# Optimization experiments

Measured on AMD Instinct MI355X. Metric: run time of the kernel, lower is better.

## Reference

```python
import jax, jax.numpy as jnp
import numpy as np

BATCH = 32768
NUM_CLASSES = 1000

def setup_inputs() -> dict:
    key = jax.random.key(0)
    k1, k2 = jax.random.split(key)
    input = jax.random.normal(k1, (BATCH, NUM_CLASSES), dtype=jnp.float32)
    target = jax.random.randint(k2, (BATCH, NUM_CLASSES), 0, 2, dtype=jnp.int32)
    return {"input": input, "target": target}

def reference(input, target):
    # LSEP: loss = log(1 + sum_{i} sum_{p in pos_i} sum_{n in neg_i} exp(x[i,n] - x[i,p]))
    # The pair sum factorizes per sample:
    #   sum_{p,n} exp(x_n - x_p) = (sum_{n in neg} exp(x_n)) * (sum_{p in pos} exp(-x_p))
    pos = target > 0
    neg = target == 0
    s_neg = jnp.sum(jnp.where(neg, jnp.exp(input), 0.0), axis=1)   # [B]
    s_pos = jnp.sum(jnp.where(pos, jnp.exp(-input), 0.0), axis=1)  # [B]
    total = jnp.sum(s_neg * s_pos)
    return jnp.log1p(total).reshape(1).astype(jnp.float32)
```

## Files before the change

### kernel.cpp

```cpp
#include <hip/hip_runtime.h>
#include <math.h>

#define BATCH   32768
#define NCLS    1000
#define NC4     250
#define NBLOCKS 2048
#define NWAVES  (NBLOCKS * 4)
#define RPW     (BATCH / NWAVES)

__device__ __forceinline__ void acc4(float4 xv, int4 tv, float& sn, float& sp) {
    float e0 = __expf(tv.x == 0 ? xv.x : -xv.x);
    float e1 = __expf(tv.y == 0 ? xv.y : -xv.y);
    float e2 = __expf(tv.z == 0 ? xv.z : -xv.z);
    float e3 = __expf(tv.w == 0 ? xv.w : -xv.w);
    sn += (tv.x == 0) ? e0 : 0.0f;  sp += (tv.x == 0) ? 0.0f : e0;
    sn += (tv.y == 0) ? e1 : 0.0f;  sp += (tv.y == 0) ? 0.0f : e1;
    sn += (tv.z == 0) ? e2 : 0.0f;  sp += (tv.z == 0) ? 0.0f : e2;
    sn += (tv.w == 0) ? e3 : 0.0f;  sp += (tv.w == 0) ? 0.0f : e3;
}

__global__ __launch_bounds__(256) void lsep_row_kernel(
    const float* __restrict__ x,
    const int*   __restrict__ t,
    float* __restrict__ wave_out) {

    const int tid   = threadIdx.x;
    const int lane  = tid & 63;
    const int gwave = blockIdx.x * 4 + (tid >> 6);

    const bool tail = (lane + 192 < NC4);

    const float4* xp = (const float4*)x + (size_t)gwave * NC4;
    const int4*   tp = (const int4*)t + (size_t)gwave * NC4;
    const size_t rstep = (size_t)NWAVES * NC4;

    float4 xv0, xv1, xv2, xv3;
    int4   tv0, tv1, tv2, tv3;

    xv0 = xp[lane];       tv0 = tp[lane];
    xv1 = xp[lane + 64];  tv1 = tp[lane + 64];
    xv2 = xp[lane + 128]; tv2 = tp[lane + 128];
    if (tail) { xv3 = xp[lane + 192]; tv3 = tp[lane + 192]; }

    float acc = 0.0f;

    #pragma unroll
    for (int r = 0; r < RPW; ++r) {
        const bool more = (r + 1 < RPW);
        const float4* xn = xp + (size_t)(r + 1) * rstep;
        const int4*   tn = tp + (size_t)(r + 1) * rstep;

        float sn = 0.0f, sp = 0.0f;

        {
            float4 xc = xv0; int4 tc = tv0;
            if (more) { xv0 = xn[lane]; tv0 = tn[lane]; }
            acc4(xc, tc, sn, sp);
        }
        {
            float4 xc = xv1; int4 tc = tv1;
            if (more) { xv1 = xn[lane + 64]; tv1 = tn[lane + 64]; }
            acc4(xc, tc, sn, sp);
        }
        {
            float4 xc = xv2; int4 tc = tv2;
            if (more) { xv2 = xn[lane + 128]; tv2 = tn[lane + 128]; }
            acc4(xc, tc, sn, sp);
        }
        if (tail) {
            float4 xc = xv3; int4 tc = tv3;
            if (more) { xv3 = xn[lane + 192]; tv3 = tn[lane + 192]; }
            acc4(xc, tc, sn, sp);
        }

        #pragma unroll
        for (int off = 32; off > 0; off >>= 1) {
            sn += __shfl_down(sn, off, 64);
            sp += __shfl_down(sp, off, 64);
        }

        if (lane == 0) acc += sn * sp;
    }

    if (lane == 0) wave_out[gwave] = acc;
}

__global__ __launch_bounds__(256) void lsep_reduce_kernel(
    const float* __restrict__ wave_out,
    float* __restrict__ out) {

    const int tid = threadIdx.x;
    const float4* r4 = (const float4*)wave_out;

    float4 a[8];
    #pragma unroll
    for (int j = 0; j < 8; ++j)
        a[j] = r4[tid + 256 * j];

    float v = 0.0f;
    #pragma unroll
    for (int j = 0; j < 8; ++j)
        v += (a[j].x + a[j].y) + (a[j].z + a[j].w);

    #pragma unroll
    for (int off = 32; off > 0; off >>= 1)
        v += __shfl_down(v, off, 64);

    __shared__ float sv[4];
    const int wave = tid >> 6;
    const int lane = tid & 63;
    if (lane == 0) sv[wave] = v;
    __syncthreads();

    if (tid == 0) {
        float total = (sv[0] + sv[1]) + (sv[2] + sv[3]);
        out[0] = log1pf(total);
    }
}

extern "C" void kernel_launch(void* const* d_in, const int* in_sizes, int n_in,
                              void* d_out, int out_size, void* d_ws, size_t ws_size,
                              hipStream_t stream) {
    const float* x = (const float*)d_in[0];
    const int*   t = (const int*)d_in[1];
    float* out     = (float*)d_out;
    float* wave_ws = (float*)d_ws;

    lsep_row_kernel<<<NBLOCKS, 256, 0, stream>>>(x, t, wave_ws);
    lsep_reduce_kernel<<<1, 256, 0, stream>>>(wave_ws, out);
}
```

Baseline: 271.2 us.

## Stream row chunks through LDS with global_load_lds and a 4-deep pipeline

Loads of input and target chunks now go directly from global memory into per-wave LDS buffers via global_load_lds. A software pipeline keeps three chunks in flight, gated by explicit s_waitcnt vmcnt counts. The aim is to raise memory-level parallelism and cut the VGPRs spent holding prefetched registers, and launch bounds now request 5 blocks per CU. In exchange it uses 32 KB of LDS per block and relies on hand-counted vmcnt waits. The code also reads LDS written by the load-to-LDS path without an explicit lgkm wait or barrier.

```diff
diff --git a/kernel.cpp b/kernel.cpp
--- a/kernel.cpp
+++ b/kernel.cpp
@@ -7,6 +7,11 @@
 #define NBLOCKS 2048
 #define NWAVES  (NBLOCKS * 4)
 #define RPW     (BATCH / NWAVES)
+
+typedef const __attribute__((address_space(1))) unsigned int gu32;
+typedef __attribute__((address_space(3)))       unsigned int lu32;
+
+#define WAITVM(N) asm volatile("s_waitcnt vmcnt(" #N ")" ::: "memory")
 
 __device__ __forceinline__ void acc4(float4 xv, int4 tv, float& sn, float& sp) {
     float e0 = __expf(tv.x == 0 ? xv.x : -xv.x);
@@ -19,68 +24,79 @@
     sn += (tv.w == 0) ? e3 : 0.0f;  sp += (tv.w == 0) ? 0.0f : e3;
 }
 
-__global__ __launch_bounds__(256) void lsep_row_kernel(
+__global__ __launch_bounds__(256, 5) void lsep_row_kernel(
     const float* __restrict__ x,
     const int*   __restrict__ t,
     float* __restrict__ wave_out) {
 
+    __shared__ __align__(16) char smem[4][4][2048];
+
     const int tid   = threadIdx.x;
     const int lane  = tid & 63;
-    const int gwave = blockIdx.x * 4 + (tid >> 6);
+    const int wv    = tid >> 6;
+    const int gwave = blockIdx.x * 4 + wv;
 
-    const bool tail = (lane + 192 < NC4);
+    auto DMA = [&](int p) {
+        const int q = p & 3;
+        if (q < 3 || lane < 58) {
+            const size_t row  = (size_t)gwave + (size_t)(p >> 2) * NWAVES;
+            const size_t cidx = row * NC4 + (size_t)(q * 64 + lane);
+            const float4* gx = (const float4*)x + cidx;
+            const int4*   gt = (const int4*)t + cidx;
+            char* sl = &smem[wv][p & 3][0];
+            __builtin_amdgcn_global_load_lds((gu32*)gx, (lu32*)sl,          16, 0, 0);
+            __builtin_amdgcn_global_load_lds((gu32*)gt, (lu32*)(sl + 1024), 16, 0, 0);
+        }
+    };
 
-    const float4* xp = (const float4*)x + (size_t)gwave * NC4;
-    const int4*   tp = (const int4*)t + (size_t)gwave * NC4;
-    const size_t rstep = (size_t)NWAVES * NC4;
-
-    float4 xv0, xv1, xv2, xv3;
-    int4   tv0, tv1, tv2, tv3;
-
-    xv0 = xp[lane];       tv0 = tp[lane];
-    xv1 = xp[lane + 64];  tv1 = tp[lane + 64];
-    xv2 = xp[lane + 128]; tv2 = tp[lane + 128];
-    if (tail) { xv3 = xp[lane + 192]; tv3 = tp[lane + 192]; }
+    auto PASS = [&](int p, float& sn, float& sp) {
+        const int q = p & 3;
+        if (q < 3 || lane < 58) {
+            const char* sl = &smem[wv][p & 3][0];
+            float4 xv = *(const float4*)(sl + lane * 16);
+            int4   tv = *(const int4*)(sl + 1024 + lane * 16);
+            acc4(xv, tv, sn, sp);
+        }
+    };
 
     float acc = 0.0f;
 
-    #pragma unroll
-    for (int r = 0; r < RPW; ++r) {
-        const bool more = (r + 1 < RPW);
-        const float4* xn = xp + (size_t)(r + 1) * rstep;
-        const int4*   tn = tp + (size_t)(r + 1) * rstep;
-
-        float sn = 0.0f, sp = 0.0f;
-
-        {
-            float4 xc = xv0; int4 tc = tv0;
-            if (more) { xv0 = xn[lane]; tv0 = tn[lane]; }
-            acc4(xc, tc, sn, sp);
-        }
-        {
-            float4 xc = xv1; int4 tc = tv1;
-            if (more) { xv1 = xn[lane + 64]; tv1 = tn[lane + 64]; }
-            acc4(xc, tc, sn, sp);
-        }
-        {
-            float4 xc = xv2; int4 tc = tv2;
-            if (more) { xv2 = xn[lane + 128]; tv2 = tn[lane + 128]; }
-            acc4(xc, tc, sn, sp);
-        }
-        if (tail) {
-            float4 xc = xv3; int4 tc = tv3;
-            if (more) { xv3 = xn[lane + 192]; tv3 = tn[lane + 192]; }
-            acc4(xc, tc, sn, sp);
-        }
-
+    auto REDUCE = [&](float sn, float sp) {
         #pragma unroll
         for (int off = 32; off > 0; off >>= 1) {
             sn += __shfl_down(sn, off, 64);
             sp += __shfl_down(sp, off, 64);
         }
+        if (lane == 0) acc += sn * sp;
+    };
 
-        if (lane == 0) acc += sn * sp;
-    }
+    DMA(0); DMA(1); DMA(2);
+
+    float sn, sp;
+    sn = 0.f; sp = 0.f;
+    DMA(3);  WAITVM(6); PASS(0, sn, sp);
+    DMA(4);  WAITVM(6); PASS(1, sn, sp);
+    DMA(5);  WAITVM(6); PASS(2, sn, sp);
+    DMA(6);  WAITVM(6); PASS(3, sn, sp);
+    REDUCE(sn, sp);
+    sn = 0.f; sp = 0.f;
+    DMA(7);  WAITVM(6); PASS(4, sn, sp);
+    DMA(8);  WAITVM(6); PASS(5, sn, sp);
+    DMA(9);  WAITVM(6); PASS(6, sn, sp);
+    DMA(10); WAITVM(6); PASS(7, sn, sp);
+    REDUCE(sn, sp);
+    sn = 0.f; sp = 0.f;
+    DMA(11); WAITVM(6); PASS(8, sn, sp);
+    DMA(12); WAITVM(6); PASS(9, sn, sp);
+    DMA(13); WAITVM(6); PASS(10, sn, sp);
+    DMA(14); WAITVM(6); PASS(11, sn, sp);
+    REDUCE(sn, sp);
+    sn = 0.f; sp = 0.f;
+    DMA(15); WAITVM(6); PASS(12, sn, sp);
+    WAITVM(4);          PASS(13, sn, sp);
+    WAITVM(2);          PASS(14, sn, sp);
+    WAITVM(0);          PASS(15, sn, sp);
+    REDUCE(sn, sp);
 
     if (lane == 0) wave_out[gwave] = acc;
 }
```

Measured after the change: 272.1 us. About the same (+0.3%).
